# Kernel optimization log

Measured on AMD Instinct MI355X. Metric: run time of the kernel, lower is better.

The kernel has to match this reference:

```python
import jax, jax.numpy as jnp
import numpy as np

NUM_CLASSES = 19  # number of distinct labels in targets (fill_max)


def setup_inputs() -> dict:
    key = jax.random.key(0)
    k1, k2 = jax.random.split(key)
    n, d = 262144, 128
    inputs = jax.random.normal(k1, (n, d), dtype=jnp.float32)
    targets = jax.random.randint(k2, (n,), 0, NUM_CLASSES, dtype=jnp.int64)
    return {"inputs": inputs, "targets": targets}


def reference(inputs, targets):
    # Same math as the O(n^2) torch loop: for each sample i, the center is the
    # mean of all samples sharing targets[i]. Computed as one segment-reduction
    # over labels followed by a gather.
    n = inputs.shape[0]
    sums = jax.ops.segment_sum(inputs, targets, num_segments=NUM_CLASSES)          # [C, d]
    counts = jax.ops.segment_sum(jnp.ones((n,), inputs.dtype), targets,
                                 num_segments=NUM_CLASSES)                          # [C]
    class_centers = sums / counts[:, None]                                          # [C, d]
    centers = class_centers[targets]                                                # [n, d]
    dist_pc = jnp.sqrt(jnp.sum((inputs - centers) ** 2, axis=1))                    # [n]
    return jnp.mean(dist_pc)
```

## Files before the change

### kernel.cpp

```cpp
#include <hip/hip_runtime.h>
#include <math.h>

#define NCLS 19
#define DIM  128
#define CD   (NCLS * DIM)
#define WPB  8
#define NBLK 256
#define NTHR 512
#define NWAVES (NBLK * WPB)
#define NRP  32
#define NLP  8
#define PPW  64

typedef float f32x4 __attribute__((ext_vector_type(4)));

__device__ __forceinline__ float4 ntload4(const float4* p) {
    f32x4 r = __builtin_nontemporal_load((const f32x4*)p);
    return make_float4(r.x, r.y, r.z, r.w);
}

template <int CTRL, int RMASK>
__device__ __forceinline__ float dpp_add(float x) {
    int t = __builtin_amdgcn_update_dpp(0, __builtin_bit_cast(int, x),
                                        CTRL, RMASK, 0xf, true);
    return x + __builtin_bit_cast(float, t);
}
__device__ __forceinline__ float reduce32_dpp(float x) {
    x = dpp_add<0x111, 0xf>(x);
    x = dpp_add<0x112, 0xf>(x);
    x = dpp_add<0x114, 0xf>(x);
    x = dpp_add<0x118, 0xf>(x);
    x = dpp_add<0x142, 0xa>(x);
    return x;
}

__device__ __forceinline__ void proc_pair(float* __restrict__ tbl,
                                          int* __restrict__ cnt,
                                          float4 v, int ca, int cb,
                                          int lane, int l31) {
    if (ca == cb) {
        v.x += __shfl_xor(v.x, 32, 64);
        v.y += __shfl_xor(v.y, 32, 64);
        v.z += __shfl_xor(v.z, 32, 64);
        v.w += __shfl_xor(v.w, 32, 64);
        float4* q = (float4*)&tbl[ca * DIM + l31 * 4];
        float4 a = *q;
        a.x += v.x; a.y += v.y; a.z += v.z; a.w += v.w;
        *q = a;
        if (lane == 0) cnt[ca] += 2;
    } else {
        int c = (lane >= 32) ? cb : ca;
        float4* q = (float4*)&tbl[c * DIM + l31 * 4];
        float4 a = *q;
        a.x += v.x; a.y += v.y; a.z += v.z; a.w += v.w;
        *q = a;
        if (lane == 0)  cnt[ca]++;
        if (lane == 32) cnt[cb]++;
    }
}

__global__ __launch_bounds__(NTHR, 2)
void k_fused(const float4* __restrict__ in4, const int* __restrict__ tgt,
             float* __restrict__ gsums, int* __restrict__ gcounts,
             int* __restrict__ bar, float* __restrict__ out,
             int npair, float inv_n) {
    __shared__ __align__(16) float ls[WPB * CD];
    __shared__ int   lcnt[WPB * NCLS];
    __shared__ float red[NTHR];
    __shared__ __align__(16) float4 holdl[WPB * NLP * 64];

    const int tid  = threadIdx.x;
    const int w    = tid >> 6;
    const int lane = tid & 63;
    const int l31  = lane & 31;
    float* tbl = &ls[w * CD];
    int*   cnt = &lcnt[w * NCLS];
    const int g = blockIdx.x * WPB + w;

    for (int i = tid; i < WPB * CD; i += NTHR) ls[i] = 0.0f;
    for (int i = tid; i < WPB * NCLS; i += NTHR) lcnt[i] = 0;
    __syncthreads();

    const bool exact = (npair == PPW * NWAVES);
    const int  lstop = exact ? (NRP + NLP) * NWAVES : 0;

    float4 hold[NRP];
    if (exact) {
        #pragma unroll
        for (int k = 0; k < NRP; k += 4) {
            const int p0 = (k + 0) * NWAVES + g;
            const int p1 = (k + 1) * NWAVES + g;
            const int p2 = (k + 2) * NWAVES + g;
            const int p3 = (k + 3) * NWAVES + g;
            float4 v0 = ntload4(&in4[(size_t)p0 * 64 + lane]);
            float4 v1 = ntload4(&in4[(size_t)p1 * 64 + lane]);
            float4 v2 = ntload4(&in4[(size_t)p2 * 64 + lane]);
            float4 v3 = ntload4(&in4[(size_t)p3 * 64 + lane]);
            int2 ab0 = *(const int2*)&tgt[2 * p0];
            int2 ab1 = *(const int2*)&tgt[2 * p1];
            int2 ab2 = *(const int2*)&tgt[2 * p2];
            int2 ab3 = *(const int2*)&tgt[2 * p3];
            hold[k + 0] = v0; hold[k + 1] = v1;
            hold[k + 2] = v2; hold[k + 3] = v3;
            proc_pair(tbl, cnt, v0, ab0.x, ab0.y, lane, l31);
            proc_pair(tbl, cnt, v1, ab1.x, ab1.y, lane, l31);
            proc_pair(tbl, cnt, v2, ab2.x, ab2.y, lane, l31);
            proc_pair(tbl, cnt, v3, ab3.x, ab3.y, lane, l31);
        }
        #pragma unroll
        for (int k = 0; k < NRP; k++) {
            asm volatile("" : "+v"(hold[k].x), "+v"(hold[k].y),
                              "+v"(hold[k].z), "+v"(hold[k].w));
        }

        float4* hbase = &holdl[(size_t)(w * NLP) * 64 + lane];
        #pragma unroll
        for (int k = 0; k < NLP; k += 4) {
            const int p0 = (NRP + k + 0) * NWAVES + g;
            const int p1 = (NRP + k + 1) * NWAVES + g;
            const int p2 = (NRP + k + 2) * NWAVES + g;
            const int p3 = (NRP + k + 3) * NWAVES + g;
            float4 v0 = ntload4(&in4[(size_t)p0 * 64 + lane]);
            float4 v1 = ntload4(&in4[(size_t)p1 * 64 + lane]);
            float4 v2 = ntload4(&in4[(size_t)p2 * 64 + lane]);
            float4 v3 = ntload4(&in4[(size_t)p3 * 64 + lane]);
            int2 ab0 = *(const int2*)&tgt[2 * p0];
            int2 ab1 = *(const int2*)&tgt[2 * p1];
            int2 ab2 = *(const int2*)&tgt[2 * p2];
            int2 ab3 = *(const int2*)&tgt[2 * p3];
            hbase[(k + 0) * 64] = v0;
            hbase[(k + 1) * 64] = v1;
            hbase[(k + 2) * 64] = v2;
            hbase[(k + 3) * 64] = v3;
            proc_pair(tbl, cnt, v0, ab0.x, ab0.y, lane, l31);
            proc_pair(tbl, cnt, v1, ab1.x, ab1.y, lane, l31);
            proc_pair(tbl, cnt, v2, ab2.x, ab2.y, lane, l31);
            proc_pair(tbl, cnt, v3, ab3.x, ab3.y, lane, l31);
        }
    }

    int p = lstop + g;
    for (; p + 3 * NWAVES < npair; p += 4 * NWAVES) {
        float4 v0 = in4[(size_t)(p             ) * 64 + lane];
        float4 v1 = in4[(size_t)(p +     NWAVES) * 64 + lane];
        float4 v2 = in4[(size_t)(p + 2 * NWAVES) * 64 + lane];
        float4 v3 = in4[(size_t)(p + 3 * NWAVES) * 64 + lane];
        int2 ab0 = *(const int2*)&tgt[2 * p];
        int2 ab1 = *(const int2*)&tgt[2 * (p + NWAVES)];
        int2 ab2 = *(const int2*)&tgt[2 * (p + 2 * NWAVES)];
        int2 ab3 = *(const int2*)&tgt[2 * (p + 3 * NWAVES)];
        proc_pair(tbl, cnt, v0, ab0.x, ab0.y, lane, l31);
        proc_pair(tbl, cnt, v1, ab1.x, ab1.y, lane, l31);
        proc_pair(tbl, cnt, v2, ab2.x, ab2.y, lane, l31);
        proc_pair(tbl, cnt, v3, ab3.x, ab3.y, lane, l31);
    }
    for (; p < npair; p += NWAVES) {
        float4 v = in4[(size_t)p * 64 + lane];
        int2 ab = *(const int2*)&tgt[2 * p];
        proc_pair(tbl, cnt, v, ab.x, ab.y, lane, l31);
    }
    __syncthreads();

    for (int i = tid; i < CD; i += NTHR) {
        float s = 0.0f;
        #pragma unroll
        for (int ww = 0; ww < WPB; ww++) s += ls[ww * CD + i];
        unsafeAtomicAdd(&gsums[i], s);
    }
    if (tid < NCLS) {
        int s = 0;
        #pragma unroll
        for (int ww = 0; ww < WPB; ww++) s += lcnt[ww * NCLS + tid];
        atomicAdd(&gcounts[tid], s);
    }

    __syncthreads();
    if (tid == 0) {
        __hip_atomic_fetch_add(bar, 1, __ATOMIC_ACQ_REL,
                               __HIP_MEMORY_SCOPE_AGENT);
        while (__hip_atomic_load(bar, __ATOMIC_ACQUIRE,
                                 __HIP_MEMORY_SCOPE_AGENT) < NBLK) {
            __builtin_amdgcn_s_sleep(8);
        }
    }
    __syncthreads();

    float* lcent = ls;
    for (int i = tid; i < CD; i += NTHR) {
        float s = __hip_atomic_load(&gsums[i], __ATOMIC_RELAXED,
                                    __HIP_MEMORY_SCOPE_AGENT);
        int   c = __hip_atomic_load(&gcounts[i >> 7], __ATOMIC_RELAXED,
                                    __HIP_MEMORY_SCOPE_AGENT);
        lcent[i] = s / (float)c;
    }
    __syncthreads();

    float acc = 0.0f;

    if (exact) {
        #pragma unroll
        for (int k = 0; k < NRP; k++) {
            const int pk = k * NWAVES + g;
            const int2 cc = *(const int2*)&tgt[2 * pk];
            const int c = (lane >= 32) ? cc.y : cc.x;
            const float4 e = *(const float4*)&lcent[c * DIM + l31 * 4];
            const float4 v = hold[k];
            float dx = v.x - e.x, dy = v.y - e.y;
            float dz = v.z - e.z, dw = v.w - e.w;
            float d = dx * dx + dy * dy + dz * dz + dw * dw;
            d = reduce32_dpp(d);
            if (l31 == 31) acc += sqrtf(d);
        }
        const float4* hbase = &holdl[(size_t)(w * NLP) * 64 + lane];
        #pragma unroll
        for (int k = 0; k < NLP; k++) {
            const int pk = (NRP + k) * NWAVES + g;
            const int2 cc = *(const int2*)&tgt[2 * pk];
            const int c = (lane >= 32) ? cc.y : cc.x;
            float4 v = hbase[k * 64];
            const float4 e = *(const float4*)&lcent[c * DIM + l31 * 4];
            float dx = v.x - e.x, dy = v.y - e.y;
            float dz = v.z - e.z, dw = v.w - e.w;
            float d = dx * dx + dy * dy + dz * dz + dw * dw;
            d = reduce32_dpp(d);
            if (l31 == 31) acc += sqrtf(d);
        }
    }

    int q = lstop + g;
    for (; q + NWAVES < npair; q += 2 * NWAVES) {
        float4 va = in4[(size_t)q * 64 + lane];
        float4 vb = in4[(size_t)(q + NWAVES) * 64 + lane];
        int2 c2a = *(const int2*)&tgt[2 * q];
        int2 c2b = *(const int2*)&tgt[2 * (q + NWAVES)];
        int ca = (lane >= 32) ? c2a.y : c2a.x;
        int cb = (lane >= 32) ? c2b.y : c2b.x;
        const float4 ea = *(const float4*)&lcent[ca * DIM + l31 * 4];
        const float4 eb = *(const float4*)&lcent[cb * DIM + l31 * 4];
        float dx, dy, dz, dw;
        dx = va.x - ea.x; dy = va.y - ea.y; dz = va.z - ea.z; dw = va.w - ea.w;
        float d0 = dx * dx + dy * dy + dz * dz + dw * dw;
        dx = vb.x - eb.x; dy = vb.y - eb.y; dz = vb.z - eb.z; dw = vb.w - eb.w;
        float d1 = dx * dx + dy * dy + dz * dz + dw * dw;
        d0 = reduce32_dpp(d0);
        d1 = reduce32_dpp(d1);
        if (l31 == 31) acc += sqrtf(d0) + sqrtf(d1);
    }
    for (; q < npair; q += NWAVES) {
        float4 v = in4[(size_t)q * 64 + lane];
        int2 c2 = *(const int2*)&tgt[2 * q];
        int c = (lane >= 32) ? c2.y : c2.x;
        const float4 e = *(const float4*)&lcent[c * DIM + l31 * 4];
        float dx = v.x - e.x, dy = v.y - e.y, dz = v.z - e.z, dw = v.w - e.w;
        float d = dx * dx + dy * dy + dz * dz + dw * dw;
        d = reduce32_dpp(d);
        if (l31 == 31) acc += sqrtf(d);
    }

    red[tid] = acc;
    __syncthreads();
    for (int s = NTHR / 2; s > 0; s >>= 1) {
        if (tid < s) red[tid] += red[tid + s];
        __syncthreads();
    }
    if (tid == 0) unsafeAtomicAdd(out, red[0] * inv_n);
}

extern "C" void kernel_launch(void* const* d_in, const int* in_sizes, int n_in,
                              void* d_out, int out_size, void* d_ws, size_t ws_size,
                              hipStream_t stream) {
    const float* in  = (const float*)d_in[0];
    const int*   tgt = (const int*)d_in[1];
    const int n = in_sizes[0] / DIM;

    float* gsums   = (float*)d_ws;
    int*   gcounts = (int*)(gsums + CD);
    int*   bar     = gcounts + NCLS;
    float* out     = (float*)d_out;

    (void)hipMemsetAsync(d_ws, 0, (CD + NCLS + 1) * sizeof(float), stream);
    (void)hipMemsetAsync(d_out, 0, sizeof(float), stream);

    const float4* in4 = (const float4*)in;
    k_fused<<<NBLK, NTHR, 0, stream>>>(in4, tgt, gsums, gcounts, bar,
                                       out, n / 2, 1.0f / (float)n);
}
```

Measured before the change: 230.3 us.

## Software-pipeline loads ahead of processing in accumulate and distance passes

Restructures the register-hold, LDS-hold and streaming loops so the next group of four rows and labels is loaded before the current group is processed, and issues all eight LDS-hold loads up front. This overlaps global memory latency with the LDS atomic and reduction work. The register-held row count is reduced to free registers for the extra in-flight values, so more rows are reloaded from global memory in the second pass.

```diff
diff --git a/kernel.cpp b/kernel.cpp
--- a/kernel.cpp
+++ b/kernel.cpp
@@ -8,7 +8,7 @@
 #define NBLK 256
 #define NTHR 512
 #define NWAVES (NBLK * WPB)
-#define NRP  32
+#define NRP  28
 #define NLP  8
 #define PPW  64
 
@@ -86,27 +86,41 @@
 
     float4 hold[NRP];
     if (exact) {
-        #pragma unroll
-        for (int k = 0; k < NRP; k += 4) {
-            const int p0 = (k + 0) * NWAVES + g;
-            const int p1 = (k + 1) * NWAVES + g;
-            const int p2 = (k + 2) * NWAVES + g;
-            const int p3 = (k + 3) * NWAVES + g;
-            float4 v0 = ntload4(&in4[(size_t)p0 * 64 + lane]);
-            float4 v1 = ntload4(&in4[(size_t)p1 * 64 + lane]);
-            float4 v2 = ntload4(&in4[(size_t)p2 * 64 + lane]);
-            float4 v3 = ntload4(&in4[(size_t)p3 * 64 + lane]);
-            int2 ab0 = *(const int2*)&tgt[2 * p0];
-            int2 ab1 = *(const int2*)&tgt[2 * p1];
-            int2 ab2 = *(const int2*)&tgt[2 * p2];
-            int2 ab3 = *(const int2*)&tgt[2 * p3];
-            hold[k + 0] = v0; hold[k + 1] = v1;
-            hold[k + 2] = v2; hold[k + 3] = v3;
-            proc_pair(tbl, cnt, v0, ab0.x, ab0.y, lane, l31);
-            proc_pair(tbl, cnt, v1, ab1.x, ab1.y, lane, l31);
-            proc_pair(tbl, cnt, v2, ab2.x, ab2.y, lane, l31);
-            proc_pair(tbl, cnt, v3, ab3.x, ab3.y, lane, l31);
-        }
+        int2 a0, a1, a2, a3;
+        {
+            const int p0 = 0 * NWAVES + g, p1 = 1 * NWAVES + g;
+            const int p2 = 2 * NWAVES + g, p3 = 3 * NWAVES + g;
+            hold[0] = ntload4(&in4[(size_t)p0 * 64 + lane]);
+            hold[1] = ntload4(&in4[(size_t)p1 * 64 + lane]);
+            hold[2] = ntload4(&in4[(size_t)p2 * 64 + lane]);
+            hold[3] = ntload4(&in4[(size_t)p3 * 64 + lane]);
+            a0 = *(const int2*)&tgt[2 * p0];
+            a1 = *(const int2*)&tgt[2 * p1];
+            a2 = *(const int2*)&tgt[2 * p2];
+            a3 = *(const int2*)&tgt[2 * p3];
+        }
+        #pragma unroll
+        for (int k = 0; k <= NRP - 8; k += 4) {
+            const int q0 = (k + 4) * NWAVES + g, q1 = (k + 5) * NWAVES + g;
+            const int q2 = (k + 6) * NWAVES + g, q3 = (k + 7) * NWAVES + g;
+            hold[k + 4] = ntload4(&in4[(size_t)q0 * 64 + lane]);
+            hold[k + 5] = ntload4(&in4[(size_t)q1 * 64 + lane]);
+            hold[k + 6] = ntload4(&in4[(size_t)q2 * 64 + lane]);
+            hold[k + 7] = ntload4(&in4[(size_t)q3 * 64 + lane]);
+            int2 b0 = *(const int2*)&tgt[2 * q0];
+            int2 b1 = *(const int2*)&tgt[2 * q1];
+            int2 b2 = *(const int2*)&tgt[2 * q2];
+            int2 b3 = *(const int2*)&tgt[2 * q3];
+            proc_pair(tbl, cnt, hold[k + 0], a0.x, a0.y, lane, l31);
+            proc_pair(tbl, cnt, hold[k + 1], a1.x, a1.y, lane, l31);
+            proc_pair(tbl, cnt, hold[k + 2], a2.x, a2.y, lane, l31);
+            proc_pair(tbl, cnt, hold[k + 3], a3.x, a3.y, lane, l31);
+            a0 = b0; a1 = b1; a2 = b2; a3 = b3;
+        }
+        proc_pair(tbl, cnt, hold[NRP - 4], a0.x, a0.y, lane, l31);
+        proc_pair(tbl, cnt, hold[NRP - 3], a1.x, a1.y, lane, l31);
+        proc_pair(tbl, cnt, hold[NRP - 2], a2.x, a2.y, lane, l31);
+        proc_pair(tbl, cnt, hold[NRP - 1], a3.x, a3.y, lane, l31);
         #pragma unroll
         for (int k = 0; k < NRP; k++) {
             asm volatile("" : "+v"(hold[k].x), "+v"(hold[k].y),
@@ -114,33 +128,44 @@
         }
 
         float4* hbase = &holdl[(size_t)(w * NLP) * 64 + lane];
-        #pragma unroll
-        for (int k = 0; k < NLP; k += 4) {
-            const int p0 = (NRP + k + 0) * NWAVES + g;
-            const int p1 = (NRP + k + 1) * NWAVES + g;
-            const int p2 = (NRP + k + 2) * NWAVES + g;
-            const int p3 = (NRP + k + 3) * NWAVES + g;
-            float4 v0 = ntload4(&in4[(size_t)p0 * 64 + lane]);
-            float4 v1 = ntload4(&in4[(size_t)p1 * 64 + lane]);
-            float4 v2 = ntload4(&in4[(size_t)p2 * 64 + lane]);
-            float4 v3 = ntload4(&in4[(size_t)p3 * 64 + lane]);
-            int2 ab0 = *(const int2*)&tgt[2 * p0];
-            int2 ab1 = *(const int2*)&tgt[2 * p1];
-            int2 ab2 = *(const int2*)&tgt[2 * p2];
-            int2 ab3 = *(const int2*)&tgt[2 * p3];
-            hbase[(k + 0) * 64] = v0;
-            hbase[(k + 1) * 64] = v1;
-            hbase[(k + 2) * 64] = v2;
-            hbase[(k + 3) * 64] = v3;
-            proc_pair(tbl, cnt, v0, ab0.x, ab0.y, lane, l31);
-            proc_pair(tbl, cnt, v1, ab1.x, ab1.y, lane, l31);
-            proc_pair(tbl, cnt, v2, ab2.x, ab2.y, lane, l31);
-            proc_pair(tbl, cnt, v3, ab3.x, ab3.y, lane, l31);
+        {
+            const int p0 = (NRP + 0) * NWAVES + g, p1 = (NRP + 1) * NWAVES + g;
+            const int p2 = (NRP + 2) * NWAVES + g, p3 = (NRP + 3) * NWAVES + g;
+            float4 c0 = ntload4(&in4[(size_t)p0 * 64 + lane]);
+            float4 c1 = ntload4(&in4[(size_t)p1 * 64 + lane]);
+            float4 c2 = ntload4(&in4[(size_t)p2 * 64 + lane]);
+            float4 c3 = ntload4(&in4[(size_t)p3 * 64 + lane]);
+            int2 d0 = *(const int2*)&tgt[2 * p0];
+            int2 d1 = *(const int2*)&tgt[2 * p1];
+            int2 d2 = *(const int2*)&tgt[2 * p2];
+            int2 d3 = *(const int2*)&tgt[2 * p3];
+            const int q0 = (NRP + 4) * NWAVES + g, q1 = (NRP + 5) * NWAVES + g;
+            const int q2 = (NRP + 6) * NWAVES + g, q3 = (NRP + 7) * NWAVES + g;
+            float4 e0 = ntload4(&in4[(size_t)q0 * 64 + lane]);
+            float4 e1 = ntload4(&in4[(size_t)q1 * 64 + lane]);
+            float4 e2 = ntload4(&in4[(size_t)q2 * 64 + lane]);
+            float4 e3 = ntload4(&in4[(size_t)q3 * 64 + lane]);
+            int2 f0 = *(const int2*)&tgt[2 * q0];
+            int2 f1 = *(const int2*)&tgt[2 * q1];
+            int2 f2 = *(const int2*)&tgt[2 * q2];
+            int2 f3 = *(const int2*)&tgt[2 * q3];
+            hbase[0 * 64] = c0; hbase[1 * 64] = c1;
+            hbase[2 * 64] = c2; hbase[3 * 64] = c3;
+            proc_pair(tbl, cnt, c0, d0.x, d0.y, lane, l31);
+            proc_pair(tbl, cnt, c1, d1.x, d1.y, lane, l31);
+            proc_pair(tbl, cnt, c2, d2.x, d2.y, lane, l31);
+            proc_pair(tbl, cnt, c3, d3.x, d3.y, lane, l31);
+            hbase[4 * 64] = e0; hbase[5 * 64] = e1;
+            hbase[6 * 64] = e2; hbase[7 * 64] = e3;
+            proc_pair(tbl, cnt, e0, f0.x, f0.y, lane, l31);
+            proc_pair(tbl, cnt, e1, f1.x, f1.y, lane, l31);
+            proc_pair(tbl, cnt, e2, f2.x, f2.y, lane, l31);
+            proc_pair(tbl, cnt, e3, f3.x, f3.y, lane, l31);
         }
     }
 
     int p = lstop + g;
-    for (; p + 3 * NWAVES < npair; p += 4 * NWAVES) {
+    if (p + 3 * NWAVES < npair) {
         float4 v0 = in4[(size_t)(p             ) * 64 + lane];
         float4 v1 = in4[(size_t)(p +     NWAVES) * 64 + lane];
         float4 v2 = in4[(size_t)(p + 2 * NWAVES) * 64 + lane];
@@ -149,10 +174,29 @@
         int2 ab1 = *(const int2*)&tgt[2 * (p + NWAVES)];
         int2 ab2 = *(const int2*)&tgt[2 * (p + 2 * NWAVES)];
         int2 ab3 = *(const int2*)&tgt[2 * (p + 3 * NWAVES)];
+        while (p + 7 * NWAVES < npair) {
+            const int pn = p + 4 * NWAVES;
+            float4 n0 = in4[(size_t)(pn             ) * 64 + lane];
+            float4 n1 = in4[(size_t)(pn +     NWAVES) * 64 + lane];
+            float4 n2 = in4[(size_t)(pn + 2 * NWAVES) * 64 + lane];
+            float4 n3 = in4[(size_t)(pn + 3 * NWAVES) * 64 + lane];
+            int2 m0 = *(const int2*)&tgt[2 * pn];
+            int2 m1 = *(const int2*)&tgt[2 * (pn + NWAVES)];
+            int2 m2 = *(const int2*)&tgt[2 * (pn + 2 * NWAVES)];
+            int2 m3 = *(const int2*)&tgt[2 * (pn + 3 * NWAVES)];
+            proc_pair(tbl, cnt, v0, ab0.x, ab0.y, lane, l31);
+            proc_pair(tbl, cnt, v1, ab1.x, ab1.y, lane, l31);
+            proc_pair(tbl, cnt, v2, ab2.x, ab2.y, lane, l31);
+            proc_pair(tbl, cnt, v3, ab3.x, ab3.y, lane, l31);
+            v0 = n0; v1 = n1; v2 = n2; v3 = n3;
+            ab0 = m0; ab1 = m1; ab2 = m2; ab3 = m3;
+            p = pn;
+        }
         proc_pair(tbl, cnt, v0, ab0.x, ab0.y, lane, l31);
         proc_pair(tbl, cnt, v1, ab1.x, ab1.y, lane, l31);
         proc_pair(tbl, cnt, v2, ab2.x, ab2.y, lane, l31);
         proc_pair(tbl, cnt, v3, ab3.x, ab3.y, lane, l31);
+        p += 4 * NWAVES;
     }
     for (; p < npair; p += NWAVES) {
         float4 v = in4[(size_t)p * 64 + lane];
@@ -228,23 +272,54 @@
     }
 
     int q = lstop + g;
-    for (; q + NWAVES < npair; q += 2 * NWAVES) {
-        float4 va = in4[(size_t)q * 64 + lane];
-        float4 vb = in4[(size_t)(q + NWAVES) * 64 + lane];
-        int2 c2a = *(const int2*)&tgt[2 * q];
-        int2 c2b = *(const int2*)&tgt[2 * (q + NWAVES)];
-        int ca = (lane >= 32) ? c2a.y : c2a.x;
-        int cb = (lane >= 32) ? c2b.y : c2b.x;
-        const float4 ea = *(const float4*)&lcent[ca * DIM + l31 * 4];
-        const float4 eb = *(const float4*)&lcent[cb * DIM + l31 * 4];
-        float dx, dy, dz, dw;
-        dx = va.x - ea.x; dy = va.y - ea.y; dz = va.z - ea.z; dw = va.w - ea.w;
-        float d0 = dx * dx + dy * dy + dz * dz + dw * dw;
-        dx = vb.x - eb.x; dy = vb.y - eb.y; dz = vb.z - eb.z; dw = vb.w - eb.w;
-        float d1 = dx * dx + dy * dy + dz * dz + dw * dw;
-        d0 = reduce32_dpp(d0);
-        d1 = reduce32_dpp(d1);
-        if (l31 == 31) acc += sqrtf(d0) + sqrtf(d1);
+    if (q + 3 * NWAVES < npair) {
+        float4 v0 = in4[(size_t)(q             ) * 64 + lane];
+        float4 v1 = in4[(size_t)(q +     NWAVES) * 64 + lane];
+        float4 v2 = in4[(size_t)(q + 2 * NWAVES) * 64 + lane];
+        float4 v3 = in4[(size_t)(q + 3 * NWAVES) * 64 + lane];
+        int2 ab0 = *(const int2*)&tgt[2 * q];
+        int2 ab1 = *(const int2*)&tgt[2 * (q + NWAVES)];
+        int2 ab2 = *(const int2*)&tgt[2 * (q + 2 * NWAVES)];
+        int2 ab3 = *(const int2*)&tgt[2 * (q + 3 * NWAVES)];
+        while (q + 7 * NWAVES < npair) {
+            const int qn = q + 4 * NWAVES;
+            float4 n0 = in4[(size_t)(qn             ) * 64 + lane];
+            float4 n1 = in4[(size_t)(qn +     NWAVES) * 64 + lane];
+            float4 n2 = in4[(size_t)(qn + 2 * NWAVES) * 64 + lane];
+            float4 n3 = in4[(size_t)(qn + 3 * NWAVES) * 64 + lane];
+            int2 m0 = *(const int2*)&tgt[2 * qn];
+            int2 m1 = *(const int2*)&tgt[2 * (qn + NWAVES)];
+            int2 m2 = *(const int2*)&tgt[2 * (qn + 2 * NWAVES)];
+            int2 m3 = *(const int2*)&tgt[2 * (qn + 3 * NWAVES)];
+            #pragma unroll
+            for (int j = 0; j < 4; j++) {
+                float4 v = (j == 0) ? v0 : (j == 1) ? v1 : (j == 2) ? v2 : v3;
+                int2  cc = (j == 0) ? ab0 : (j == 1) ? ab1 : (j == 2) ? ab2 : ab3;
+                int c = (lane >= 32) ? cc.y : cc.x;
+                const float4 e = *(const float4*)&lcent[c * DIM + l31 * 4];
+                float dx = v.x - e.x, dy = v.y - e.y;
+                float dz = v.z - e.z, dw = v.w - e.w;
+                float d = dx * dx + dy * dy + dz * dz + dw * dw;
+                d = reduce32_dpp(d);
+                if (l31 == 31) acc += sqrtf(d);
+            }
+            v0 = n0; v1 = n1; v2 = n2; v3 = n3;
+            ab0 = m0; ab1 = m1; ab2 = m2; ab3 = m3;
+            q = qn;
+        }
+        #pragma unroll
+        for (int j = 0; j < 4; j++) {
+            float4 v = (j == 0) ? v0 : (j == 1) ? v1 : (j == 2) ? v2 : v3;
+            int2  cc = (j == 0) ? ab0 : (j == 1) ? ab1 : (j == 2) ? ab2 : ab3;
+            int c = (lane >= 32) ? cc.y : cc.x;
+            const float4 e = *(const float4*)&lcent[c * DIM + l31 * 4];
+            float dx = v.x - e.x, dy = v.y - e.y;
+            float dz = v.z - e.z, dw = v.w - e.w;
+            float d = dx * dx + dy * dy + dz * dz + dw * dw;
+            d = reduce32_dpp(d);
+            if (l31 == 31) acc += sqrtf(d);
+        }
+        q += 4 * NWAVES;
     }
     for (; q < npair; q += NWAVES) {
         float4 v = in4[(size_t)q * 64 + lane];
```

Result: faster. 222.3 us, median of 2 (-3.5%).
